# Kernel tuning notes

Measured on AMD Instinct MI355X. Metric: run time of the kernel, lower is better.

## Reference

```python
import jax, jax.numpy as jnp
import numpy as np

WS = 7
SHIFT = 3
NH = 6


def _rel_index(ws):
    coords = np.stack(np.meshgrid(np.arange(ws), np.arange(ws), indexing='ij'))  # (2, ws, ws)
    cf = coords.reshape(2, -1)                       # (2, N)
    rel = (cf[:, :, None] - cf[:, None, :]).transpose(1, 2, 0).copy()  # (N, N, 2)
    rel[:, :, 0] += ws - 1
    rel[:, :, 1] += ws - 1
    rel[:, :, 0] *= 2 * ws - 1
    return rel.sum(-1)                               # (N, N) int


def _attn_mask(Hp, Wp, ws, shift):
    img = np.zeros((Hp, Wp))
    cnt = 0
    sl = (slice(0, -ws), slice(-ws, -shift), slice(-shift, None))
    for h in sl:
        for w in sl:
            img[h, w] = cnt
            cnt += 1
    mw = img.reshape(Hp // ws, ws, Wp // ws, ws).transpose(0, 2, 1, 3).reshape(-1, ws * ws)
    am = mw[:, None, :] - mw[:, :, None]
    return np.where(am != 0, -100.0, 0.0).astype(np.float32)  # (num_win, N, N)


def _ln(x, g, b, eps=1e-5):
    m = x.mean(-1, keepdims=True)
    v = ((x - m) ** 2).mean(-1, keepdims=True)
    return (x - m) * jax.lax.rsqrt(v + eps) * g + b


def _forward(x, qkv_w, qkv_b, proj_w, proj_b, rpb_table,
             norm1_g, norm1_b, norm2_g, norm2_b,
             mlp_w1, mlp_b1, mlp_w2, mlp_b2, H, W):
    B, L, C = x.shape
    ws, nh = WS, NH
    hd = C // nh
    N = ws * ws
    shortcut = x

    h = _ln(x, norm1_g, norm1_b).reshape(B, H, W, C)
    pad_b = (ws - H % ws) % ws
    pad_r = (ws - W % ws) % ws
    if pad_b or pad_r:
        h = jnp.pad(h, ((0, 0), (0, pad_b), (0, pad_r), (0, 0)))
    Hp, Wp = H + pad_b, W + pad_r
    shift = SHIFT if min(Hp, Wp) > ws else 0
    if shift:
        h = jnp.roll(h, (-shift, -shift), axis=(1, 2))

    nwh, nww = Hp // ws, Wp // ws
    # window partition -> (B*num_win, N, C)
    win = h.reshape(B, nwh, ws, nww, ws, C).transpose(0, 1, 3, 2, 4, 5).reshape(-1, N, C)

    qkv = (win @ qkv_w.T + qkv_b).reshape(-1, N, 3, nh, hd).transpose(2, 0, 3, 1, 4)
    q, k, v = qkv[0], qkv[1], qkv[2]          # (BW, nh, N, hd)
    attn = jnp.einsum('bhnd,bhmd->bhnm', q, k) * (hd ** -0.5)

    ridx = _rel_index(ws)
    bias = rpb_table[ridx.reshape(-1)].reshape(N, N, nh).transpose(2, 0, 1)  # (nh, N, N)
    attn = attn + bias[None]

    if shift:
        m = jnp.asarray(_attn_mask(Hp, Wp, ws, shift))  # (num_win, N, N)
        nw = nwh * nww
        attn = attn.reshape(B, nw, nh, N, N) + m[None, :, None]
        attn = attn.reshape(-1, nh, N, N)

    attn = jax.nn.softmax(attn, axis=-1)
    out = jnp.einsum('bhnm,bhmd->bnhd', attn, v).reshape(-1, N, C)
    out = out @ proj_w.T + proj_b

    # window reverse -> (B, Hp, Wp, C)
    out = out.reshape(B, nwh, nww, ws, ws, C).transpose(0, 1, 3, 2, 4, 5).reshape(B, Hp, Wp, C)
    if shift:
        out = jnp.roll(out, (shift, shift), axis=(1, 2))
    out = out[:, :H, :W].reshape(B, H * W, C)

    x = shortcut + out
    h2 = _ln(x, norm2_g, norm2_b)
    h2 = jax.nn.gelu(h2 @ mlp_w1.T + mlp_b1, approximate=False) @ mlp_w2.T + mlp_b2
    return x + h2


def setup_inputs() -> dict:
    key = jax.random.key(0)
    ks = jax.random.split(key, 8)
    B, H, W, C = 32, 56, 56, 192
    hid = 4 * C
    s = 0.02
    return {
        'x': jax.random.normal(ks[0], (B, H * W, C), jnp.float32),
        'qkv_w': jax.random.normal(ks[1], (3 * C, C), jnp.float32) * s,
        'qkv_b': jnp.zeros((3 * C,), jnp.float32),
        'proj_w': jax.random.normal(ks[2], (C, C), jnp.float32) * s,
        'proj_b': jnp.zeros((C,), jnp.float32),
        'rpb_table': jax.random.normal(ks[3], ((2 * WS - 1) ** 2, NH), jnp.float32) * s,
        'norm1_g': jnp.ones((C,), jnp.float32),
        'norm1_b': jnp.zeros((C,), jnp.float32),
        'norm2_g': jnp.ones((C,), jnp.float32),
        'norm2_b': jnp.zeros((C,), jnp.float32),
        'mlp_w1': jax.random.normal(ks[4], (hid, C), jnp.float32) * s,
        'mlp_b1': jnp.zeros((hid,), jnp.float32),
        'mlp_w2': jax.random.normal(ks[5], (C, hid), jnp.float32) * s,
        'mlp_b2': jnp.zeros((C,), jnp.float32),
        'H': H,
        'W': W,
    }


def reference(x, qkv_w, qkv_b, proj_w, proj_b, rpb_table,
              norm1_g, norm1_b, norm2_g, norm2_b,
              mlp_w1, mlp_b1, mlp_w2, mlp_b2, H, W):
    return _forward(x, qkv_w, qkv_b, proj_w, proj_b, rpb_table,
                    norm1_g, norm1_b, norm2_g, norm2_b,
                    mlp_w1, mlp_b1, mlp_w2, mlp_b2, int(H), int(W))
```

## Files before the change

kernel.cpp:

```cpp
#include <hip/hip_runtime.h>
#include <hip/hip_bf16.h>
#include <math.h>

typedef short short8 __attribute__((ext_vector_type(8)));
typedef float floatx4 __attribute__((ext_vector_type(4)));

__device__ __forceinline__ void async16(const void* g, void* l) {
  __builtin_amdgcn_global_load_lds((const __attribute__((address_space(1))) void*)g,
                                   (__attribute__((address_space(3))) void*)l, 16, 0, 0);
}

__global__ void cvt_kernel(const float* __restrict__ in, __hip_bfloat16* __restrict__ o, int n) {
  int i = blockIdx.x * 256 + threadIdx.x;
  if (i < n) o[i] = __float2bfloat16(in[i]);
}

__global__ void table_kernel(const float* __restrict__ rpb, float* __restrict__ tb) {
  int i = blockIdx.x * 256 + threadIdx.x;
  if (i >= 4 * 6 * 64 * 64) return;
  int n = i & 63, m = (i >> 6) & 63;
  int hc = i >> 12, head = hc % 6, cls = hc / 6;
  float v;
  if (m >= 49 || n >= 49) {
    v = -30000.0f;
  } else {
    int rm = m / 7, cm = m - rm * 7;
    int rn = n / 7, cn = n - rn * 7;
    float bias = rpb[((rm - rn + 6) * 13 + (cm - cn + 6)) * 6 + head];
    int regm = ((cls & 2) ? (rm < 4 ? 1 : 2) : 0) * 3 + ((cls & 1) ? (cm < 4 ? 1 : 2) : 0);
    int regn = ((cls & 2) ? (rn < 4 ? 1 : 2) : 0) * 3 + ((cls & 1) ? (cn < 4 ? 1 : 2) : 0);
    v = bias + (regm != regn ? -100.0f : 0.0f);
  }
  tb[i] = v;
}

template<bool WINDOWED>
__global__ __launch_bounds__(256) void ln_kernel(const float* __restrict__ x,
                                                 const float* __restrict__ g,
                                                 const float* __restrict__ b,
                                                 __hip_bfloat16* __restrict__ out) {
  int w = threadIdx.x >> 6, lane = threadIdx.x & 63;
  int row = blockIdx.x * 4 + w;
  size_t src_row;
  if (WINDOWED) {
    int wi = row / 49, t = row - wi * 49;
    int bb = wi >> 6, wim = wi & 63, wh = wim >> 3, wwn = wim & 7;
    int r = t / 7, c = t - r * 7;
    int y = wh * 7 + r + 3;  if (y >= 56) y -= 56;
    int xp = wwn * 7 + c + 3; if (xp >= 56) xp -= 56;
    src_row = (size_t)bb * 3136 + (size_t)y * 56 + xp;
  } else {
    src_row = row;
  }
  const float* src = x + src_row * 192;
  float v0 = src[lane], v1 = src[lane + 64], v2 = src[lane + 128];
  float s = v0 + v1 + v2;
#pragma unroll
  for (int off = 32; off > 0; off >>= 1) s += __shfl_xor(s, off, 64);
  float mean = s * (1.0f / 192.0f);
  float d0 = v0 - mean, d1 = v1 - mean, d2 = v2 - mean;
  float q = d0 * d0 + d1 * d1 + d2 * d2;
#pragma unroll
  for (int off = 32; off > 0; off >>= 1) q += __shfl_xor(q, off, 64);
  float rstd = rsqrtf(q * (1.0f / 192.0f) + 1e-5f);
  __hip_bfloat16* o = out + (size_t)row * 192;
  o[lane]       = __float2bfloat16(d0 * rstd * g[lane]       + b[lane]);
  o[lane + 64]  = __float2bfloat16(d1 * rstd * g[lane + 64]  + b[lane + 64]);
  o[lane + 128] = __float2bfloat16(d2 * rstd * g[lane + 128] + b[lane + 128]);
}

template<int K, int EPI>
__global__ __launch_bounds__(256) void gemm_bt(const __hip_bfloat16* __restrict__ A,
                                               const __hip_bfloat16* __restrict__ B,
                                               const float* __restrict__ bias,
                                               const float* residF,
                                               float* outF,
                                               __hip_bfloat16* __restrict__ outB,
                                               int N) {
  __shared__ __hip_bfloat16 sA[128 * 64];
  __shared__ __hip_bfloat16 sB[64 * 64];
  const int m0 = blockIdx.y * 128;
  const int n0 = blockIdx.x * 64;
  const int tid = threadIdx.x;
  const int w = tid >> 6, lane = tid & 63;
  const int quad = lane >> 4, l16 = lane & 15;
  const int wr = w >> 1, wc = w & 1;

  floatx4 acc[4][2] = {};

  const __hip_bfloat16* Abase = A + (size_t)m0 * K;
  const __hip_bfloat16* Bbase = B + (size_t)n0 * K;

  for (int k0 = 0; k0 < K; k0 += 64) {
    const __hip_bfloat16* Ag = Abase + k0;
#pragma unroll
    for (int it = 0; it < 4; ++it) {
      int cb = ((it * 4 + w) << 6);
      int c = cb + lane;
      async16(Ag + (size_t)(c >> 3) * K + ((c & 7) << 3), &sA[cb * 8]);
    }
    const __hip_bfloat16* Bg = Bbase + k0;
#pragma unroll
    for (int it = 0; it < 2; ++it) {
      int cb = ((it * 4 + w) << 6);
      int c = cb + lane;
      async16(Bg + (size_t)(c >> 3) * K + ((c & 7) << 3), &sB[cb * 8]);
    }
    __syncthreads();

#pragma unroll
    for (int kk = 0; kk < 64; kk += 32) {
      short8 af[4], bf[2];
#pragma unroll
      for (int ri = 0; ri < 4; ++ri)
        af[ri] = *(const short8*)&sA[(wr * 64 + ri * 16 + l16) * 64 + kk + quad * 8];
#pragma unroll
      for (int ci = 0; ci < 2; ++ci)
        bf[ci] = *(const short8*)&sB[(wc * 32 + ci * 16 + l16) * 64 + kk + quad * 8];
#pragma unroll
      for (int ri = 0; ri < 4; ++ri)
#pragma unroll
        for (int ci = 0; ci < 2; ++ci)
          acc[ri][ci] = __builtin_amdgcn_mfma_f32_16x16x32_bf16(af[ri], bf[ci], acc[ri][ci], 0, 0, 0);
    }
    __syncthreads();
  }

  const int m_base = m0 + wr * 64;
#pragma unroll
  for (int ri = 0; ri < 4; ++ri) {
#pragma unroll
    for (int ci = 0; ci < 2; ++ci) {
      const int ccol = n0 + wc * 32 + ci * 16 + l16;
      const float bv = bias[ccol];
#pragma unroll
      for (int reg = 0; reg < 4; ++reg) {
        const int row = m_base + ri * 16 + quad * 4 + reg;
        float v = acc[ri][ci][reg] + bv;
        if (EPI == 0) {
          outB[(size_t)row * N + ccol] = __float2bfloat16(v);
        } else if (EPI == 1) {
          int wi = row / 49, t = row - wi * 49;
          int bb = wi >> 6, wim = wi & 63, wh = wim >> 3, wwn = wim & 7;
          int r = t / 7, c = t - r * 7;
          int y = wh * 7 + r + 3;  if (y >= 56) y -= 56;
          int xp = wwn * 7 + c + 3; if (xp >= 56) xp -= 56;
          size_t drow = ((size_t)bb * 3136 + (size_t)y * 56 + xp) * 192 + ccol;
          outF[drow] = v + residF[drow];
        } else if (EPI == 2) {
          float gl = 0.5f * v * (1.0f + erff(v * 0.70710678118654752f));
          outB[(size_t)row * N + ccol] = __float2bfloat16(gl);
        } else {
          size_t o = (size_t)row * 192 + ccol;
          outF[o] = v + residF[o];
        }
      }
    }
  }
}

__global__ __launch_bounds__(256) void attn_kernel(const __hip_bfloat16* __restrict__ qkv,
                                                   const float* __restrict__ table,
                                                   __hip_bfloat16* __restrict__ out) {
  __shared__ __hip_bfloat16 Plds[4][64 * 72];
  __shared__ __hip_bfloat16 Vt[4][32 * 64];
  const int slot = threadIdx.x >> 6, lane = threadIdx.x & 63;
  const int quad = lane >> 4, l16 = lane & 15;

  const int wg = blockIdx.x * 4 + slot;
  const int wi = wg / 6, head = wg - wi * 6;
  const int wim = wi & 63, wh = wim >> 3, wwn = wim & 7;
  const int cls = ((wh == 7) ? 2 : 0) + ((wwn == 7) ? 1 : 0);
  const __hip_bfloat16* base = qkv + (size_t)wi * 49 * 576 + head * 32;

  const __hip_bfloat16* vbase = base + 384;
#pragma unroll
  for (int it = 0; it < 4; ++it) {
    int p = it * 64 + lane;
    if (p < 196) {
      int k = p >> 2, c = p & 3;
      short8 sv = *(const short8*)(vbase + k * 576 + c * 8);
#pragma unroll
      for (int j = 0; j < 8; ++j)
        Vt[slot][(c * 8 + j) * 64 + k] = ((const __hip_bfloat16*)&sv)[j];
    }
  }
#pragma unroll
  for (int it = 0; it < 8; ++it) {
    int p = it * 64 + lane;
    if (p < 480) {
      int k = 49 + (p >> 5), n = p & 31;
      Vt[slot][n * 64 + k] = __float2bfloat16(0.0f);
    }
  }

  short8 aq[4], bk[4];
#pragma unroll
  for (int t = 0; t < 4; ++t) {
    int m = l16 + 16 * t; if (m > 48) m = 48;
    aq[t] = *(const short8*)(base + m * 576 + quad * 8);
    bk[t] = *(const short8*)(base + 192 + m * 576 + quad * 8);
  }

  floatx4 sc[4][4] = {};
#pragma unroll
  for (int ti = 0; ti < 4; ++ti)
#pragma unroll
    for (int tj = 0; tj < 4; ++tj)
      sc[ti][tj] = __builtin_amdgcn_mfma_f32_16x16x32_bf16(aq[ti], bk[tj], sc[ti][tj], 0, 0, 0);

  const float scale = 0.17677669529663689f;
  const float* tb = table + (((size_t)cls * 6 + head) << 12);
  float linv[4][4];
#pragma unroll
  for (int ti = 0; ti < 4; ++ti) {
#pragma unroll
    for (int r = 0; r < 4; ++r) {
      const int row = 16 * ti + quad * 4 + r;
      const float* trow = tb + row * 64 + l16;
      float v0 = sc[ti][0][r] * scale + trow[0];
      float v1 = sc[ti][1][r] * scale + trow[16];
      float v2 = sc[ti][2][r] * scale + trow[32];
      float v3 = sc[ti][3][r] * scale + trow[48];
      float mx = fmaxf(fmaxf(v0, v1), fmaxf(v2, v3));
      mx = fmaxf(mx, __shfl_xor(mx, 1));
      mx = fmaxf(mx, __shfl_xor(mx, 2));
      mx = fmaxf(mx, __shfl_xor(mx, 4));
      mx = fmaxf(mx, __shfl_xor(mx, 8));
      v0 = __expf(v0 - mx); v1 = __expf(v1 - mx);
      v2 = __expf(v2 - mx); v3 = __expf(v3 - mx);
      float sm = (v0 + v1) + (v2 + v3);
      sm += __shfl_xor(sm, 1);
      sm += __shfl_xor(sm, 2);
      sm += __shfl_xor(sm, 4);
      sm += __shfl_xor(sm, 8);
      linv[ti][r] = 1.0f / sm;
      __hip_bfloat16* pr = &Plds[slot][row * 72 + l16];
      pr[0]  = __float2bfloat16(v0);
      pr[16] = __float2bfloat16(v1);
      pr[32] = __float2bfloat16(v2);
      pr[48] = __float2bfloat16(v3);
    }
  }
  __syncthreads();

  floatx4 oc[4][2] = {};
#pragma unroll
  for (int kb = 0; kb < 64; kb += 32) {
    short8 ap[4], bv[2];
#pragma unroll
    for (int ti = 0; ti < 4; ++ti)
      ap[ti] = *(const short8*)&Plds[slot][(l16 + 16 * ti) * 72 + kb + quad * 8];
#pragma unroll
    for (int t2 = 0; t2 < 2; ++t2)
      bv[t2] = *(const short8*)&Vt[slot][(l16 + 16 * t2) * 64 + kb + quad * 8];
#pragma unroll
    for (int ti = 0; ti < 4; ++ti)
#pragma unroll
      for (int t2 = 0; t2 < 2; ++t2)
        oc[ti][t2] = __builtin_amdgcn_mfma_f32_16x16x32_bf16(ap[ti], bv[t2], oc[ti][t2], 0, 0, 0);
  }

#pragma unroll
  for (int ti = 0; ti < 4; ++ti) {
#pragma unroll
    for (int reg = 0; reg < 4; ++reg) {
      const int row = 16 * ti + quad * 4 + reg;
      if (row < 49) {
        __hip_bfloat16* op = out + ((size_t)wi * 49 + row) * 192 + head * 32 + l16;
        const float li = linv[ti][reg];
        op[0]  = __float2bfloat16(oc[ti][0][reg] * li);
        op[16] = __float2bfloat16(oc[ti][1][reg] * li);
      }
    }
  }
}

extern "C" void kernel_launch(void* const* d_in, const int* in_sizes, int n_in,
                              void* d_out, int out_size, void* d_ws, size_t ws_size,
                              hipStream_t stream) {
  const float* x      = (const float*)d_in[0];
  const float* qkv_w  = (const float*)d_in[1];
  const float* qkv_b  = (const float*)d_in[2];
  const float* proj_w = (const float*)d_in[3];
  const float* proj_b = (const float*)d_in[4];
  const float* rpb    = (const float*)d_in[5];
  const float* n1g    = (const float*)d_in[6];
  const float* n1b    = (const float*)d_in[7];
  const float* n2g    = (const float*)d_in[8];
  const float* n2b    = (const float*)d_in[9];
  const float* w1     = (const float*)d_in[10];
  const float* b1     = (const float*)d_in[11];
  const float* w2     = (const float*)d_in[12];
  const float* b2     = (const float*)d_in[13];
  float* out = (float*)d_out;

  char* ws = (char*)d_ws;
  __hip_bfloat16* bufB = (__hip_bfloat16*)ws;
  __hip_bfloat16* bufA = (__hip_bfloat16*)(ws + 154140672);
  __hip_bfloat16* wqb = (__hip_bfloat16*)(ws + 154140672 + 38535168);
  __hip_bfloat16* wpb = wqb + 110592;
  __hip_bfloat16* w1b = wpb + 36864;
  __hip_bfloat16* w2b = w1b + 147456;
  float* tablef = (float*)(ws + 154140672 + 38535168 + 884736);

  cvt_kernel<<<(110592 + 255) / 256, 256, 0, stream>>>(qkv_w, wqb, 110592);
  cvt_kernel<<<(36864  + 255) / 256, 256, 0, stream>>>(proj_w, wpb, 36864);
  cvt_kernel<<<(147456 + 255) / 256, 256, 0, stream>>>(w1, w1b, 147456);
  cvt_kernel<<<(147456 + 255) / 256, 256, 0, stream>>>(w2, w2b, 147456);
  table_kernel<<<384, 256, 0, stream>>>(rpb, tablef);

  ln_kernel<true><<<25088, 256, 0, stream>>>(x, n1g, n1b, bufA);
  gemm_bt<192, 0><<<dim3(9, 784), 256, 0, stream>>>(bufA, wqb, qkv_b, nullptr, nullptr, bufB, 576);
  attn_kernel<<<3072, 256, 0, stream>>>(bufB, tablef, bufA);
  gemm_bt<192, 1><<<dim3(3, 784), 256, 0, stream>>>(bufA, wpb, proj_b, x, out, nullptr, 192);
  ln_kernel<false><<<25088, 256, 0, stream>>>(out, n2g, n2b, bufA);
  gemm_bt<192, 2><<<dim3(12, 784), 256, 0, stream>>>(bufA, w1b, b1, nullptr, nullptr, bufB, 768);
  gemm_bt<768, 3><<<dim3(3, 784), 256, 0, stream>>>(bufB, w2b, b2, out, out, nullptr, 192);
}
```

Baseline: 544.0 us.

## Fuse MLP fc1+GELU+fc2 into one kernel keeping hidden activations on-chip

Replaces the two MLP GEMM launches with a single kernel. Each 64-row block loops over the 768-wide hidden dimension in chunks of 32, computing fc1 plus GELU into LDS and accumulating fc2 straight into registers. This avoids writing and re-reading the large bf16 hidden activation buffer in global memory, which also lets the workspace shrink. The cost is that W1 and W2 are re-streamed for every row block, and each 32-wide chunk needs several barriers, which may limit MFMA utilization.

```diff
diff --git a/kernel.cpp b/kernel.cpp
--- a/kernel.cpp
+++ b/kernel.cpp
@@ -139,7 +139,7 @@
         float v = acc[ri][ci][reg] + bv;
         if (EPI == 0) {
           outB[(size_t)row * N + ccol] = __float2bfloat16(v);
-        } else if (EPI == 1) {
+        } else {
           int wi = row / 49, t = row - wi * 49;
           int bb = wi >> 6, wim = wi & 63, wh = wim >> 3, wwn = wim & 7;
           int r = t / 7, c = t - r * 7;
@@ -147,13 +147,100 @@
           int xp = wwn * 7 + c + 3; if (xp >= 56) xp -= 56;
           size_t drow = ((size_t)bb * 3136 + (size_t)y * 56 + xp) * 192 + ccol;
           outF[drow] = v + residF[drow];
-        } else if (EPI == 2) {
-          float gl = 0.5f * v * (1.0f + erff(v * 0.70710678118654752f));
-          outB[(size_t)row * N + ccol] = __float2bfloat16(gl);
-        } else {
-          size_t o = (size_t)row * 192 + ccol;
-          outF[o] = v + residF[o];
         }
+      }
+    }
+  }
+}
+
+__global__ __launch_bounds__(256, 3) void mlp_kernel(const __hip_bfloat16* __restrict__ A,
+                                                     const __hip_bfloat16* __restrict__ W1,
+                                                     const float* __restrict__ b1,
+                                                     const __hip_bfloat16* __restrict__ W2,
+                                                     const float* __restrict__ b2,
+                                                     float* __restrict__ out) {
+  __shared__ __hip_bfloat16 sW1[32 * 192];
+  __shared__ __hip_bfloat16 sW2[192 * 32];
+  __shared__ __hip_bfloat16 sH[64 * 40];
+  const int tid = threadIdx.x;
+  const int w = tid >> 6, lane = tid & 63;
+  const int quad = lane >> 4, l16 = lane & 15;
+  const int wr = w >> 1, wc = w & 1;
+  const size_t rowblk = (size_t)blockIdx.x * 64;
+
+  short8 af[6];
+  {
+    const __hip_bfloat16* arow = A + (rowblk + w * 16 + l16) * 192 + quad * 8;
+#pragma unroll
+    for (int j = 0; j < 6; ++j) af[j] = *(const short8*)(arow + 32 * j);
+  }
+
+  floatx4 acc[2][6] = {};
+
+  for (int hb = 0; hb < 768; hb += 32) {
+    __syncthreads();
+    {
+      const char* s1 = (const char*)(W1 + hb * 192);
+#pragma unroll
+      for (int it = 0; it < 3; ++it) {
+        int c = it * 256 + tid;
+        async16(s1 + c * 16, (char*)sW1 + c * 16);
+      }
+      const char* s2 = (const char*)W2 + hb * 2;
+#pragma unroll
+      for (int it = 0; it < 3; ++it) {
+        int c = it * 256 + tid;
+        async16(s2 + (size_t)(c >> 2) * 1536 + (c & 3) * 16, (char*)sW2 + c * 16);
+      }
+    }
+    __syncthreads();
+
+    floatx4 hc[2] = {};
+#pragma unroll
+    for (int j = 0; j < 6; ++j) {
+#pragma unroll
+      for (int t = 0; t < 2; ++t) {
+        short8 bw = *(const short8*)&sW1[(t * 16 + l16) * 192 + j * 32 + quad * 8];
+        hc[t] = __builtin_amdgcn_mfma_f32_16x16x32_bf16(af[j], bw, hc[t], 0, 0, 0);
+      }
+    }
+#pragma unroll
+    for (int t = 0; t < 2; ++t) {
+      const float bv = b1[hb + t * 16 + l16];
+#pragma unroll
+      for (int r = 0; r < 4; ++r) {
+        float v = hc[t][r] + bv;
+        float g = 0.5f * v * (1.0f + erff(v * 0.70710678118654752f));
+        sH[(w * 16 + quad * 4 + r) * 40 + t * 16 + l16] = __float2bfloat16(g);
+      }
+    }
+    __syncthreads();
+
+    short8 ah[2], bw2[6];
+#pragma unroll
+    for (int mi = 0; mi < 2; ++mi)
+      ah[mi] = *(const short8*)&sH[(wr * 32 + mi * 16 + l16) * 40 + quad * 8];
+#pragma unroll
+    for (int ni = 0; ni < 6; ++ni)
+      bw2[ni] = *(const short8*)&sW2[(wc * 96 + ni * 16 + l16) * 32 + quad * 8];
+#pragma unroll
+    for (int mi = 0; mi < 2; ++mi)
+#pragma unroll
+      for (int ni = 0; ni < 6; ++ni)
+        acc[mi][ni] = __builtin_amdgcn_mfma_f32_16x16x32_bf16(ah[mi], bw2[ni], acc[mi][ni], 0, 0, 0);
+  }
+
+#pragma unroll
+  for (int mi = 0; mi < 2; ++mi) {
+#pragma unroll
+    for (int ni = 0; ni < 6; ++ni) {
+      const int ccol = wc * 96 + ni * 16 + l16;
+      const float bv = b2[ccol];
+#pragma unroll
+      for (int r = 0; r < 4; ++r) {
+        const size_t row = rowblk + wr * 32 + mi * 16 + quad * 4 + r;
+        float* p = out + row * 192 + ccol;
+        *p = *p + acc[mi][ni][r] + bv;
       }
     }
   }
@@ -297,12 +384,12 @@
 
   char* ws = (char*)d_ws;
   __hip_bfloat16* bufB = (__hip_bfloat16*)ws;
-  __hip_bfloat16* bufA = (__hip_bfloat16*)(ws + 154140672);
-  __hip_bfloat16* wqb = (__hip_bfloat16*)(ws + 154140672 + 38535168);
+  __hip_bfloat16* bufA = (__hip_bfloat16*)(ws + 115605504);
+  __hip_bfloat16* wqb = (__hip_bfloat16*)(ws + 115605504 + 38535168);
   __hip_bfloat16* wpb = wqb + 110592;
   __hip_bfloat16* w1b = wpb + 36864;
   __hip_bfloat16* w2b = w1b + 147456;
-  float* tablef = (float*)(ws + 154140672 + 38535168 + 884736);
+  float* tablef = (float*)(ws + 115605504 + 38535168 + 884736);
 
   cvt_kernel<<<(110592 + 255) / 256, 256, 0, stream>>>(qkv_w, wqb, 110592);
   cvt_kernel<<<(36864  + 255) / 256, 256, 0, stream>>>(proj_w, wpb, 36864);
@@ -315,6 +402,5 @@
   attn_kernel<<<3072, 256, 0, stream>>>(bufB, tablef, bufA);
   gemm_bt<192, 1><<<dim3(3, 784), 256, 0, stream>>>(bufA, wpb, proj_b, x, out, nullptr, 192);
   ln_kernel<false><<<25088, 256, 0, stream>>>(out, n2g, n2b, bufA);
-  gemm_bt<192, 2><<<dim3(12, 784), 256, 0, stream>>>(bufA, w1b, b1, nullptr, nullptr, bufB, 768);
-  gemm_bt<768, 3><<<dim3(3, 784), 256, 0, stream>>>(bufB, w2b, b2, out, out, nullptr, 192);
-}
+  mlp_kernel<<<1568, 256, 0, stream>>>(bufA, w1b, b1, w2b, b2, out);
+}
```

Result: faster. 522.8 us (-3.9%).
